# Kernel tuning notes

Measured on AMD Instinct MI355X. Metric: run time of the kernel, lower is better.

## Reference

```python
import jax, jax.numpy as jnp
import numpy as np

B, T, S, H, V = 8, 1024, 1024, 1024, 5000


def setup_inputs() -> dict:
    key = jax.random.key(0)
    ks = jax.random.split(key, 9)
    x = jax.random.normal(ks[0], (B, T, H), dtype=jnp.float32)
    encoder_attn_w = jax.random.uniform(ks[1], (B, T, S), dtype=jnp.float32)
    # normalize like attention weights over source dim
    encoder_attn_w = encoder_attn_w / jnp.sum(encoder_attn_w, axis=-1, keepdims=True)
    nodes = jax.random.randint(ks[2], (B, S), 0, V)
    scale = 0.02
    Wg = jax.random.normal(ks[3], (H, 1), dtype=jnp.float32) * scale
    bg = jnp.zeros((1,), dtype=jnp.float32)
    Wf = jax.random.normal(ks[4], (H, H), dtype=jnp.float32) * scale
    bf = jnp.zeros((H,), dtype=jnp.float32)
    Wv = jax.random.normal(ks[5], (H, V), dtype=jnp.float32) * scale
    bv = jnp.zeros((V,), dtype=jnp.float32)
    return {"x": x, "encoder_attn_w": encoder_attn_w, "nodes": nodes,
            "Wg": Wg, "bg": bg, "Wf": Wf, "bf": bf, "Wv": Wv, "bv": bv}


def reference(x, encoder_attn_w, nodes, Wg, bg, Wf, bf, Wv, bv):
    # Conv1D == affine along last dim (GPT-2 style): x @ W + b
    p_gen = jax.nn.sigmoid(x @ Wg + bg)                      # [B,T,1]
    h = jax.nn.gelu(x @ Wf + bf)                             # fc with activation
    logits = h @ Wv + bv                                     # [B,T,V]
    out = jax.nn.softmax(logits, axis=-1) * p_gen            # gated generate dist
    # pointer/copy: scatter-add attention mass (1 - p_gen) into vocab slots
    add = encoder_attn_w * (1.0 - p_gen)                     # [B,T,S]
    b_idx = jnp.arange(B)[:, None, None]
    t_idx = jnp.arange(T)[None, :, None]
    v_idx = jnp.broadcast_to(nodes[:, None, :], (B, T, S))
    out = out.at[b_idx, t_idx, v_idx].add(add)
    return out
```

## Files before the change

### kernel.cpp

```cpp
#include <hip/hip_runtime.h>

#define Mq   8192
#define Hq   1024
#define Sq   1024
#define Tq   1024
#define Vq   5000
#define Vpad 5120

typedef __bf16 bf16;
typedef bf16  bf16x8 __attribute__((ext_vector_type(8)));
typedef bf16  bf16x4 __attribute__((ext_vector_type(4)));
typedef float f32x4  __attribute__((ext_vector_type(4)));

typedef const __attribute__((address_space(1))) void* gas_t;
typedef __attribute__((address_space(3))) void*       sas_t;

__device__ __forceinline__ void async_copy16(const void* g, void* s) {
  __builtin_amdgcn_global_load_lds((gas_t)g, (sas_t)s, 16, 0, 0);
}

__global__ __launch_bounds__(256) void pgen_cvt(
    const float* __restrict__ x, const float* __restrict__ Wg,
    const float* __restrict__ bg, bf16* __restrict__ xb,
    float* __restrict__ pgen) {
  const int m = blockIdx.x;
  const int t = threadIdx.x;
  float4 v = ((const float4*)(x + (size_t)m * Hq))[t];
  float4 g = ((const float4*)Wg)[t];
  float dot = v.x * g.x + v.y * g.y + v.z * g.z + v.w * g.w;
  bf16x4 o;
  o[0] = (bf16)v.x; o[1] = (bf16)v.y; o[2] = (bf16)v.z; o[3] = (bf16)v.w;
  ((bf16x4*)(xb + (size_t)m * Hq))[t] = o;
  #pragma unroll
  for (int off = 32; off; off >>= 1) dot += __shfl_down(dot, off, 64);
  __shared__ float red[4];
  if ((t & 63) == 0) red[t >> 6] = dot;
  __syncthreads();
  if (t == 0) {
    float s = red[0] + red[1] + red[2] + red[3] + bg[0];
    pgen[m] = 1.0f / (1.0f + __expf(-s));
  }
}

__global__ __launch_bounds__(256) void transpose_cvt(
    const float* __restrict__ W, bf16* __restrict__ WT,
    int K, int Nin, int Npad) {
  __shared__ float tile[32][33];
  const int nb = blockIdx.x * 32, kb = blockIdx.y * 32;
  const int tx = threadIdx.x, ty = threadIdx.y;
  #pragma unroll
  for (int i = 0; i < 32; i += 8) {
    int k = kb + ty + i, n = nb + tx;
    tile[ty + i][tx] = (n < Nin) ? W[(size_t)k * Nin + n] : 0.0f;
  }
  __syncthreads();
  #pragma unroll
  for (int i = 0; i < 32; i += 8) {
    int n = nb + ty + i, k = kb + tx;
    if (n < Npad) WT[(size_t)n * K + k] = (bf16)tile[tx][ty + i];
  }
}

template <int MODE>
__global__ __launch_bounds__(256, 2) void gemm_mfma(
    const bf16* __restrict__ A, const bf16* __restrict__ BT,
    const float* __restrict__ bias, float* __restrict__ outF,
    bf16* __restrict__ outB, int M, int N, int K, int Nstore) {
  __shared__ bf16 As[2][128 * 32];
  __shared__ bf16 Bs[2][128 * 32];
  const int tid  = threadIdx.x;
  const int w    = tid >> 6;
  const int l    = tid & 63;
  const int quad = l >> 4;
  const int t16  = l & 15;
  const int wm   = (w >> 1) * 64;
  const int wn   = (w & 1) * 64;
  const int m0   = blockIdx.x * 128;
  const int n0   = blockIdx.y * 128;
  const int srow = l >> 2;
  const int scol = (l & 3) * 8;

  f32x4 acc[4][4] = {};

  const int row0 = (w * 16) + srow;
  const int row1 = ((4 + w) * 16) + srow;
  const bf16* aP0 = A  + (size_t)(m0 + row0) * K + scol;
  const bf16* aP1 = A  + (size_t)(m0 + row1) * K + scol;
  const bf16* bP0 = BT + (size_t)(n0 + row0) * K + scol;
  const bf16* bP1 = BT + (size_t)(n0 + row1) * K + scol;
  const int ldsOff0 = (w)     * 512;
  const int ldsOff1 = (4 + w) * 512;

  async_copy16(aP0, As[0] + ldsOff0);
  async_copy16(bP0, Bs[0] + ldsOff0);
  async_copy16(aP1, As[0] + ldsOff1);
  async_copy16(bP1, Bs[0] + ldsOff1);
  __syncthreads();

  int cur = 0;
  for (int k0 = 0; k0 < K; k0 += 32) {
    if (k0 + 32 < K) {
      const int nxt = cur ^ 1;
      async_copy16(aP0 + k0 + 32, As[nxt] + ldsOff0);
      async_copy16(bP0 + k0 + 32, Bs[nxt] + ldsOff0);
      async_copy16(aP1 + k0 + 32, As[nxt] + ldsOff1);
      async_copy16(bP1 + k0 + 32, Bs[nxt] + ldsOff1);
    }

    bf16x8 af[4], bfr[4];
    #pragma unroll
    for (int i = 0; i < 4; ++i)
      af[i] = *(const bf16x8*)(As[cur] + (wm + 16 * i + t16) * 32 + quad * 8);
    #pragma unroll
    for (int j = 0; j < 4; ++j)
      bfr[j] = *(const bf16x8*)(Bs[cur] + (wn + 16 * j + t16) * 32 + quad * 8);
    #pragma unroll
    for (int i = 0; i < 4; ++i)
      #pragma unroll
      for (int j = 0; j < 4; ++j)
        acc[i][j] = __builtin_amdgcn_mfma_f32_16x16x32_bf16(bfr[j], af[i], acc[i][j], 0, 0, 0);

    __syncthreads();
    cur ^= 1;
  }

  #pragma unroll
  for (int j = 0; j < 4; ++j) {
    const int nb = n0 + wn + 16 * j + quad * 4;
    float4 bj4 = make_float4(0.0f, 0.0f, 0.0f, 0.0f);
    if (MODE == 0 || nb < Nstore) bj4 = *(const float4*)(bias + nb);
    #pragma unroll
    for (int i = 0; i < 4; ++i) {
      const int mg = m0 + wm + 16 * i + t16;
      float v0 = acc[i][j][0] + bj4.x;
      float v1 = acc[i][j][1] + bj4.y;
      float v2 = acc[i][j][2] + bj4.z;
      float v3 = acc[i][j][3] + bj4.w;
      if (MODE == 0) {
        bf16x4 o;
        float vv[4] = {v0, v1, v2, v3};
        #pragma unroll
        for (int r = 0; r < 4; ++r) {
          float v  = vv[r];
          float u  = 0.7978845608028654f * (v + 0.044715f * v * v * v);
          float e2 = __expf(2.0f * u);
          float th = 1.0f - 2.0f / (e2 + 1.0f);
          o[r] = (bf16)(0.5f * v * (1.0f + th));
        }
        *(bf16x4*)(outB + (size_t)mg * N + nb) = o;
      } else if (MODE == 1) {
        if (nb < Nstore) {
          bf16x4 o;
          o[0] = (bf16)__expf(v0); o[1] = (bf16)__expf(v1);
          o[2] = (bf16)__expf(v2); o[3] = (bf16)__expf(v3);
          *(bf16x4*)(outB + (size_t)mg * Nstore + nb) = o;
        }
      } else {
        if (nb < Nstore) {
          float4 o = make_float4(__expf(v0), __expf(v1), __expf(v2), __expf(v3));
          *(float4*)(outF + (size_t)mg * Nstore + nb) = o;
        }
      }
    }
  }
}

template <typename ET>
__global__ __launch_bounds__(256) void finalize(
    float* __restrict__ out, const ET* __restrict__ e,
    const float* __restrict__ pgen, const float* __restrict__ attn,
    const int* __restrict__ nodes) {
  const int m = blockIdx.x;
  const int b = m / Tq;
  const int t = threadIdx.x;
  __shared__ float buf[Vq];
  __shared__ float red[4];

  float s = 0.0f;
  const ET* erow = e + (size_t)m * Vq;
  if constexpr (sizeof(ET) == 2) {
    const bf16x8* e8 = (const bf16x8*)erow;
    for (int i = t; i < Vq / 8; i += 256) {
      bf16x8 v = e8[i];
      #pragma unroll
      for (int k = 0; k < 8; ++k) {
        float f = (float)v[k];
        buf[i * 8 + k] = f;
        s += f;
      }
    }
  } else {
    const float4* e4 = (const float4*)erow;
    for (int i = t; i < Vq / 4; i += 256) {
      float4 v = e4[i];
      buf[i * 4 + 0] = v.x; buf[i * 4 + 1] = v.y;
      buf[i * 4 + 2] = v.z; buf[i * 4 + 3] = v.w;
      s += (v.x + v.y) + (v.z + v.w);
    }
  }
  #pragma unroll
  for (int off = 32; off; off >>= 1) s += __shfl_down(s, off, 64);
  if ((t & 63) == 0) red[t >> 6] = s;
  __syncthreads();
  s = red[0] + red[1] + red[2] + red[3];

  const float pg    = pgen[m];
  const float scale = pg / s;
  const float coef  = (1.0f - pg) / scale;

  const float* arow = attn + (size_t)m * Sq;
  const int*   nrow = nodes + (size_t)b * Sq;
  for (int sIdx = t; sIdx < Sq; sIdx += 256)
    atomicAdd(&buf[nrow[sIdx]], arow[sIdx] * coef);
  __syncthreads();

  float4* o4 = (float4*)(out + (size_t)m * Vq);
  const float4* b4 = (const float4*)buf;
  for (int i = t; i < Vq / 4; i += 256) {
    float4 v = b4[i];
    v.x *= scale; v.y *= scale; v.z *= scale; v.w *= scale;
    o4[i] = v;
  }
}

extern "C" void kernel_launch(void* const* d_in, const int* in_sizes, int n_in,
                              void* d_out, int out_size, void* d_ws, size_t ws_size,
                              hipStream_t stream) {
  const float* x    = (const float*)d_in[0];
  const float* attn = (const float*)d_in[1];
  const int*   nodes= (const int*)d_in[2];
  const float* Wg   = (const float*)d_in[3];
  const float* bg   = (const float*)d_in[4];
  const float* Wf   = (const float*)d_in[5];
  const float* bf_  = (const float*)d_in[6];
  const float* Wv   = (const float*)d_in[7];
  const float* bv   = (const float*)d_in[8];
  float* out = (float*)d_out;

  char* w = (char*)d_ws;

  const size_t NEED = 111312896ull;
  const bool big = ws_size >= NEED;

  if (big) {
    bf16*  eB   = (bf16*)(w);
    bf16*  xb   = (bf16*)(w);
    bf16*  hB   = (bf16*)(w + 81920000ull);
    bf16*  WfT  = (bf16*)(w + 98697216ull);
    bf16*  WvT  = (bf16*)(w + 100794368ull);
    float* pgen = (float*)(w + 111280128ull);

    pgen_cvt<<<Mq, 256, 0, stream>>>(x, Wg, bg, xb, pgen);
    transpose_cvt<<<dim3(Hq / 32, Hq / 32), dim3(32, 8), 0, stream>>>(Wf, WfT, Hq, Hq, Hq);
    transpose_cvt<<<dim3(Vpad / 32, Hq / 32), dim3(32, 8), 0, stream>>>(Wv, WvT, Hq, Vq, Vpad);
    gemm_mfma<0><<<dim3(Mq / 128, Hq / 128), 256, 0, stream>>>(
        xb, WfT, bf_, nullptr, hB, Mq, Hq, Hq, Hq);
    gemm_mfma<1><<<dim3(Mq / 128, Vpad / 128), 256, 0, stream>>>(
        hB, WvT, bv, nullptr, eB, Mq, Vpad, Hq, Vq);
    finalize<bf16><<<Mq, 256, 0, stream>>>(out, eB, pgen, attn, nodes);
  } else {
    bf16*  xb   = (bf16*)(w);
    bf16*  hB   = (bf16*)(w + 16777216);
    bf16*  WfT  = (bf16*)(w + 33554432);
    bf16*  WvT  = (bf16*)(w + 35651584);
    float* pgen = (float*)(w + 46137344);

    pgen_cvt<<<Mq, 256, 0, stream>>>(x, Wg, bg, xb, pgen);
    transpose_cvt<<<dim3(Hq / 32, Hq / 32), dim3(32, 8), 0, stream>>>(Wf, WfT, Hq, Hq, Hq);
    transpose_cvt<<<dim3(Vpad / 32, Hq / 32), dim3(32, 8), 0, stream>>>(Wv, WvT, Hq, Vq, Vpad);
    gemm_mfma<0><<<dim3(Mq / 128, Hq / 128), 256, 0, stream>>>(
        xb, WfT, bf_, nullptr, hB, Mq, Hq, Hq, Hq);
    gemm_mfma<2><<<dim3(Mq / 128, Vpad / 128), 256, 0, stream>>>(
        hB, WvT, bv, out, nullptr, Mq, Vpad, Hq, Vq);
    finalize<float><<<Mq, 256, 0, stream>>>(out, out, pgen, attn, nodes);
  }
}
```

Measured before the change: 431.7 us.

## Rework pgen and finalize kernels, split vocab GEMM into two halves

pgen_cvt now assigns one wavefront per row, four rows per block, which drops the LDS reduction and the block barrier. The bf16 finalize becomes a 512-thread kernel that holds the exp values in registers and keeps only the scatter buffer in LDS, with the attention loads issued early. The vocab GEMM is launched as two half-M launches. This lowers LDS traffic and barrier cost in finalize, but the split GEMM adds a launch and may cost some tail efficiency.

```diff
diff --git a/kernel.cpp b/kernel.cpp
--- a/kernel.cpp
+++ b/kernel.cpp
@@ -23,23 +23,24 @@
     const float* __restrict__ x, const float* __restrict__ Wg,
     const float* __restrict__ bg, bf16* __restrict__ xb,
     float* __restrict__ pgen) {
-  const int m = blockIdx.x;
-  const int t = threadIdx.x;
-  float4 v = ((const float4*)(x + (size_t)m * Hq))[t];
-  float4 g = ((const float4*)Wg)[t];
-  float dot = v.x * g.x + v.y * g.y + v.z * g.z + v.w * g.w;
-  bf16x4 o;
-  o[0] = (bf16)v.x; o[1] = (bf16)v.y; o[2] = (bf16)v.z; o[3] = (bf16)v.w;
-  ((bf16x4*)(xb + (size_t)m * Hq))[t] = o;
+  const int m    = blockIdx.x * 4 + (threadIdx.x >> 6);
+  const int lane = threadIdx.x & 63;
+  const float4* xr = (const float4*)(x + (size_t)m * Hq);
+  const float4* gr = (const float4*)Wg;
+  bf16x4* xo = (bf16x4*)(xb + (size_t)m * Hq);
+  float dot = 0.0f;
+  #pragma unroll
+  for (int k = 0; k < 4; ++k) {
+    float4 v = xr[lane + 64 * k];
+    float4 g = gr[lane + 64 * k];
+    dot += v.x * g.x + v.y * g.y + v.z * g.z + v.w * g.w;
+    bf16x4 o;
+    o[0] = (bf16)v.x; o[1] = (bf16)v.y; o[2] = (bf16)v.z; o[3] = (bf16)v.w;
+    xo[lane + 64 * k] = o;
+  }
   #pragma unroll
   for (int off = 32; off; off >>= 1) dot += __shfl_down(dot, off, 64);
-  __shared__ float red[4];
-  if ((t & 63) == 0) red[t >> 6] = dot;
-  __syncthreads();
-  if (t == 0) {
-    float s = red[0] + red[1] + red[2] + red[3] + bg[0];
-    pgen[m] = 1.0f / (1.0f + __expf(-s));
-  }
+  if (lane == 0) pgen[m] = 1.0f / (1.0f + __expf(-(dot + bg[0])));
 }
 
 __global__ __launch_bounds__(256) void transpose_cvt(
@@ -137,8 +138,8 @@
       float v2 = acc[i][j][2] + bj4.z;
       float v3 = acc[i][j][3] + bj4.w;
       if (MODE == 0) {
+        float vv[4] = {v0, v1, v2, v3};
         bf16x4 o;
-        float vv[4] = {v0, v1, v2, v3};
         #pragma unroll
         for (int r = 0; r < 4; ++r) {
           float v  = vv[r];
@@ -165,9 +166,94 @@
   }
 }
 
-template <typename ET>
-__global__ __launch_bounds__(256) void finalize(
-    float* __restrict__ out, const ET* __restrict__ e,
+__global__ __launch_bounds__(512) void finalize2(
+    float* __restrict__ out, const bf16* __restrict__ e,
+    const float* __restrict__ pgen, const float* __restrict__ attn,
+    const int* __restrict__ nodes) {
+  const int m = blockIdx.x;
+  const int b = m >> 10;
+  const int t = threadIdx.x;
+  __shared__ float buf[Vq];
+  __shared__ float red[8];
+
+  float4* b4 = (float4*)buf;
+  #pragma unroll
+  for (int k = 0; k < 3; ++k) {
+    int i = t + 512 * k;
+    if (i < Vq / 4) b4[i] = make_float4(0.0f, 0.0f, 0.0f, 0.0f);
+  }
+
+  const float pg = pgen[m];
+  const float* arow = attn + (size_t)m * Sq;
+  const int*   nrow = nodes + (size_t)b * Sq;
+  const float a0 = arow[t];
+  const float a1 = arow[t + 512];
+  const int   n0i = nrow[t];
+  const int   n1i = nrow[t + 512];
+
+  const bf16x8* e8 = (const bf16x8*)(e + (size_t)m * Vq);
+  const bf16x8 ev0 = e8[t];
+  const bool   has1 = (t < 113);
+  bf16x8 ev1 = {};
+  if (has1) ev1 = e8[512 + t];
+
+  float s = 0.0f;
+  float f0[8], f1[8];
+  #pragma unroll
+  for (int k = 0; k < 8; ++k) { f0[k] = (float)ev0[k]; s += f0[k]; }
+  #pragma unroll
+  for (int k = 0; k < 8; ++k) { f1[k] = (float)ev1[k]; }
+  if (has1) {
+    #pragma unroll
+    for (int k = 0; k < 8; ++k) s += f1[k];
+  }
+  #pragma unroll
+  for (int off = 32; off; off >>= 1) s += __shfl_down(s, off, 64);
+  if ((t & 63) == 0) red[t >> 6] = s;
+
+  __syncthreads();
+
+  const float ci = 1.0f - pg;
+  atomicAdd(&buf[n0i], a0 * ci);
+  atomicAdd(&buf[n1i], a1 * ci);
+
+  float S = 0.0f;
+  #pragma unroll
+  for (int k = 0; k < 8; ++k) S += red[k];
+  const float scale = pg / S;
+
+  __syncthreads();
+
+  float4* o4 = (float4*)(out + (size_t)m * Vq);
+  {
+    float4 lo = make_float4(f0[0] * scale + buf[t * 8 + 0],
+                            f0[1] * scale + buf[t * 8 + 1],
+                            f0[2] * scale + buf[t * 8 + 2],
+                            f0[3] * scale + buf[t * 8 + 3]);
+    float4 hi = make_float4(f0[4] * scale + buf[t * 8 + 4],
+                            f0[5] * scale + buf[t * 8 + 5],
+                            f0[6] * scale + buf[t * 8 + 6],
+                            f0[7] * scale + buf[t * 8 + 7]);
+    o4[2 * t]     = lo;
+    o4[2 * t + 1] = hi;
+  }
+  if (has1) {
+    const int base = (512 + t) * 8;
+    float4 lo = make_float4(f1[0] * scale + buf[base + 0],
+                            f1[1] * scale + buf[base + 1],
+                            f1[2] * scale + buf[base + 2],
+                            f1[3] * scale + buf[base + 3]);
+    float4 hi = make_float4(f1[4] * scale + buf[base + 4],
+                            f1[5] * scale + buf[base + 5],
+                            f1[6] * scale + buf[base + 6],
+                            f1[7] * scale + buf[base + 7]);
+    o4[2 * (512 + t)]     = lo;
+    o4[2 * (512 + t) + 1] = hi;
+  }
+}
+
+__global__ __launch_bounds__(256) void finalize_f32(
+    float* __restrict__ out, const float* __restrict__ e,
     const float* __restrict__ pgen, const float* __restrict__ attn,
     const int* __restrict__ nodes) {
   const int m = blockIdx.x;
@@ -177,26 +263,13 @@
   __shared__ float red[4];
 
   float s = 0.0f;
-  const ET* erow = e + (size_t)m * Vq;
-  if constexpr (sizeof(ET) == 2) {
-    const bf16x8* e8 = (const bf16x8*)erow;
-    for (int i = t; i < Vq / 8; i += 256) {
-      bf16x8 v = e8[i];
-      #pragma unroll
-      for (int k = 0; k < 8; ++k) {
-        float f = (float)v[k];
-        buf[i * 8 + k] = f;
-        s += f;
-      }
-    }
-  } else {
-    const float4* e4 = (const float4*)erow;
-    for (int i = t; i < Vq / 4; i += 256) {
-      float4 v = e4[i];
-      buf[i * 4 + 0] = v.x; buf[i * 4 + 1] = v.y;
-      buf[i * 4 + 2] = v.z; buf[i * 4 + 3] = v.w;
-      s += (v.x + v.y) + (v.z + v.w);
-    }
+  const float* erow = e + (size_t)m * Vq;
+  const float4* e4 = (const float4*)erow;
+  float4* b4w = (float4*)buf;
+  for (int i = t; i < Vq / 4; i += 256) {
+    float4 v = e4[i];
+    b4w[i] = v;
+    s += (v.x + v.y) + (v.z + v.w);
   }
   #pragma unroll
   for (int off = 32; off; off >>= 1) s += __shfl_down(s, off, 64);
@@ -250,14 +323,17 @@
     bf16*  WvT  = (bf16*)(w + 100794368ull);
     float* pgen = (float*)(w + 111280128ull);
 
-    pgen_cvt<<<Mq, 256, 0, stream>>>(x, Wg, bg, xb, pgen);
+    pgen_cvt<<<Mq / 4, 256, 0, stream>>>(x, Wg, bg, xb, pgen);
     transpose_cvt<<<dim3(Hq / 32, Hq / 32), dim3(32, 8), 0, stream>>>(Wf, WfT, Hq, Hq, Hq);
     transpose_cvt<<<dim3(Vpad / 32, Hq / 32), dim3(32, 8), 0, stream>>>(Wv, WvT, Hq, Vq, Vpad);
     gemm_mfma<0><<<dim3(Mq / 128, Hq / 128), 256, 0, stream>>>(
         xb, WfT, bf_, nullptr, hB, Mq, Hq, Hq, Hq);
-    gemm_mfma<1><<<dim3(Mq / 128, Vpad / 128), 256, 0, stream>>>(
-        hB, WvT, bv, nullptr, eB, Mq, Vpad, Hq, Vq);
-    finalize<bf16><<<Mq, 256, 0, stream>>>(out, eB, pgen, attn, nodes);
+    gemm_mfma<1><<<dim3(Mq / 256, Vpad / 128), 256, 0, stream>>>(
+        hB, WvT, bv, nullptr, eB, Mq / 2, Vpad, Hq, Vq);
+    gemm_mfma<1><<<dim3(Mq / 256, Vpad / 128), 256, 0, stream>>>(
+        hB + (size_t)(Mq / 2) * Hq, WvT, bv, nullptr,
+        eB + (size_t)(Mq / 2) * Vq, Mq / 2, Vpad, Hq, Vq);
+    finalize2<<<Mq, 512, 0, stream>>>(out, eB, pgen, attn, nodes);
   } else {
     bf16*  xb   = (bf16*)(w);
     bf16*  hB   = (bf16*)(w + 16777216);
@@ -265,13 +341,13 @@
     bf16*  WvT  = (bf16*)(w + 35651584);
     float* pgen = (float*)(w + 46137344);
 
-    pgen_cvt<<<Mq, 256, 0, stream>>>(x, Wg, bg, xb, pgen);
+    pgen_cvt<<<Mq / 4, 256, 0, stream>>>(x, Wg, bg, xb, pgen);
     transpose_cvt<<<dim3(Hq / 32, Hq / 32), dim3(32, 8), 0, stream>>>(Wf, WfT, Hq, Hq, Hq);
     transpose_cvt<<<dim3(Vpad / 32, Hq / 32), dim3(32, 8), 0, stream>>>(Wv, WvT, Hq, Vq, Vpad);
     gemm_mfma<0><<<dim3(Mq / 128, Hq / 128), 256, 0, stream>>>(
         xb, WfT, bf_, nullptr, hB, Mq, Hq, Hq, Hq);
     gemm_mfma<2><<<dim3(Mq / 128, Vpad / 128), 256, 0, stream>>>(
         hB, WvT, bv, out, nullptr, Mq, Vpad, Hq, Vq);
-    finalize<float><<<Mq, 256, 0, stream>>>(out, out, pgen, attn, nodes);
-  }
-}
+    finalize_f32<<<Mq, 256, 0, stream>>>(out, out, pgen, attn, nodes);
+  }
+}
```

After: 442.4 us. +2.5%, slower.
